# Performance work log

Hardware: AMD Instinct MI355X
Metric: run time of the kernel (lower is better)

Reference implementation:

```python
import jax, jax.numpy as jnp
import numpy as np

USER_NUM, ITEM_NUM, D, E, B = 50000, 20000, 64, 2_000_000, 16384
N = USER_NUM + ITEM_NUM


def setup_inputs() -> dict:
    key = jax.random.key(0)
    ks = jax.random.split(key, 20)
    return {
        "user_emb": jax.random.normal(ks[0], (USER_NUM, D), jnp.float32),
        "item_emb": jax.random.normal(ks[1], (ITEM_NUM, D), jnp.float32),
        "edge_row": jax.random.randint(ks[2], (E,), 0, N, jnp.int32),
        "edge_col": jax.random.randint(ks[3], (E,), 0, N, jnp.int32),
        "edge_val": jax.random.uniform(ks[4], (E,), jnp.float32),
        "Wg1": jax.random.normal(ks[5], (D, D), jnp.float32) * 0.05,
        "bg1": jax.random.normal(ks[6], (D,), jnp.float32) * 0.05,
        "Wg2": jax.random.normal(ks[7], (D, D), jnp.float32) * 0.05,
        "bg2": jax.random.normal(ks[8], (D,), jnp.float32) * 0.05,
        "W1": jax.random.normal(ks[9], (4 * D, D), jnp.float32) * 0.05,
        "b1": jax.random.normal(ks[10], (D,), jnp.float32) * 0.05,
        "W2": jax.random.normal(ks[11], (D, 32), jnp.float32) * 0.05,
        "b2": jax.random.normal(ks[12], (32,), jnp.float32) * 0.05,
        "W3": jax.random.normal(ks[13], (32, 1), jnp.float32) * 0.05,
        "b3": jax.random.normal(ks[14], (1,), jnp.float32) * 0.05,
        "userID": jax.random.randint(ks[15], (B,), 0, USER_NUM, jnp.int32),
        "itemID": jax.random.randint(ks[16], (B,), 0, ITEM_NUM, jnp.int32),
    }


def _spmm(row, col, val, x):
    # sparse [N,N] @ dense [N,D] via gather + segment_sum
    msgs = val[:, None] * x[col]  # [E, D]
    return jax.ops.segment_sum(msgs, row, num_segments=N)


def reference(user_emb, item_emb, edge_row, edge_col, edge_val,
              Wg1, bg1, Wg2, bg2, W1, b1, W2, b2, W3, b3, userID, itemID):
    features = jnp.concatenate([user_emb, item_emb], axis=0)  # [N, D]
    final = features
    # single GCN layer (layers=[64,64]); L1 = L + I so SpMM(L1,x) = SpMM(L,x) + x
    lx = _spmm(edge_row, edge_col, edge_val, features)
    lx2 = _spmm(edge_row, edge_col, edge_val, features * features)
    inter1 = (lx + features) @ Wg1 + bg1
    inter2 = lx2 @ Wg2 + bg2
    h = jax.nn.leaky_relu(inter1 + inter2, negative_slope=0.01)
    final = jnp.concatenate([final, h], axis=1)  # [N, 2D]

    u = final[userID]                     # [B, 2D]
    i = final[itemID + USER_NUM]          # [B, 2D]
    embed = jnp.concatenate([u, i], axis=1)  # [B, 4D]
    embed = jax.nn.relu(embed @ W1 + b1)
    embed = jax.nn.relu(embed @ W2 + b2)
    embed = embed @ W3 + b3
    return embed.reshape(-1)
```

## Files before the change

kernel.cpp:

```cpp
#include <hip/hip_runtime.h>
#include <hip/hip_bf16.h>

#define USER_NUM 50000
#define ITEM_NUM 20000
#define NNODE    70000
#define DD       64
#define CHUNK    1024
#define NCHUNK   ((NNODE + CHUNK - 1) / CHUNK)
#define GROWS    (NNODE / 8)
#define APB      2048
#define EPT      8
#define NS2      128
#define NB3      16
#define T_CAP    32768
#define NCHUNK2  (T_CAP / CHUNK)
#define GCAP     327680
#define RT       16

__device__ __forceinline__ const float* feat_row(const float* __restrict__ ue,
                                                 const float* __restrict__ ie, int n) {
    return (n < USER_NUM) ? (ue + (size_t)n * DD)
                          : (ie + (size_t)(n - USER_NUM) * DD);
}


__global__ __launch_bounds__(256) void zero_kernel(int* __restrict__ cnt2,
                                                   int* __restrict__ tmask,
                                                   int* __restrict__ gcur) {
    const int tid    = blockIdx.x * 256 + (int)threadIdx.x;
    const int stride = gridDim.x * 256;
    for (int i = tid; i < T_CAP; i += stride) cnt2[i] = 0;
    for (int i = tid; i < NNODE; i += stride) tmask[i] = 0;
    if (tid < 8) gcur[tid] = tid * GCAP;
}


__global__ __launch_bounds__(256) void mark_kernel(const int* __restrict__ uid,
                                                   const int* __restrict__ iid,
                                                   int* __restrict__ tmask, int B) {
    const int stride = gridDim.x * blockDim.x;
    for (int s = blockIdx.x * blockDim.x + threadIdx.x; s < B; s += stride) {
        tmask[uid[s]] = 1;
        tmask[USER_NUM + iid[s]] = 1;
    }
}


__global__ __launch_bounds__(256) void chunksum_kernel(const int* __restrict__ arr,
                                                       int* __restrict__ csum, int N) {
    __shared__ int red[4];
    const int c = blockIdx.x;
    const int t = threadIdx.x;
    int s = 0;
#pragma unroll
    for (int i = 0; i < 4; ++i) {
        const int idx = c * CHUNK + t + 256 * i;
        s += (idx < N) ? arr[idx] : 0;
    }
#pragma unroll
    for (int off = 32; off; off >>= 1) s += __shfl_down(s, off);
    if ((t & 63) == 0) red[t >> 6] = s;
    __syncthreads();
    if (t == 0) csum[c] = red[0] + red[1] + red[2] + red[3];
}

__global__ __launch_bounds__(128) void scan_small_kernel(const int* __restrict__ csum,
                                                         int* __restrict__ coff,
                                                         int NC) {
    __shared__ int s[128];
    const int t = threadIdx.x;
    const int v = (t < NC) ? csum[t] : 0;
    s[t] = v;
    __syncthreads();
    for (int off = 1; off < 128; off <<= 1) {
        const int val = s[t];
        const int add = (t >= off) ? s[t - off] : 0;
        __syncthreads();
        s[t] = val + add;
        __syncthreads();
    }
    if (t < NC) coff[t] = s[t] - v;
}

__global__ __launch_bounds__(256) void fill_flags_kernel(
    const int* __restrict__ tmask, const int* __restrict__ coff,
    int* __restrict__ cmapx, int* __restrict__ nodes, int* __restrict__ meta,
    int* __restrict__ gslot) {
    __shared__ int sp[256];
    const int c  = blockIdx.x;
    const int t  = threadIdx.x;
    const int g0 = c * CHUNK + t * 4;
    int v[4];
#pragma unroll
    for (int i = 0; i < 4; ++i) v[i] = (g0 + i < NNODE) ? tmask[g0 + i] : 0;
    const int s = ((v[0] + v[1]) + (v[2] + v[3]));
    sp[t] = s;
    __syncthreads();
    for (int off = 1; off < 256; off <<= 1) {
        const int val = sp[t];
        const int add = (t >= off) ? sp[t - off] : 0;
        __syncthreads();
        sp[t] = val + add;
        __syncthreads();
    }
    int run = coff[c] + sp[t] - s;
#pragma unroll
    for (int i = 0; i < 4; ++i) {
        const int g = g0 + i;
        if (g < NNODE) {
            cmapx[g] = v[i] ? run : -1;
            if (v[i]) nodes[run] = g;
            if (g == USER_NUM) meta[1] = run;
            if (g % GROWS == 0) gslot[g / GROWS] = run;
            run += v[i];
        } else if (g == NNODE) {
            meta[0] = run;
            gslot[8] = run;
        }
    }
    if (g0 + 4 == NNODE) { meta[0] = run; gslot[8] = run; }
}

__global__ __launch_bounds__(256) void fill_kernel(const int* __restrict__ cnt,
                                                   const int* __restrict__ coff,
                                                   int* __restrict__ base,
                                                   int* __restrict__ cursor, int N) {
    __shared__ int sp[256];
    const int c  = blockIdx.x;
    const int t  = threadIdx.x;
    const int g0 = c * CHUNK + t * 4;
    int v[4];
#pragma unroll
    for (int i = 0; i < 4; ++i) v[i] = (g0 + i < N) ? cnt[g0 + i] : 0;
    const int s = ((v[0] + v[1]) + (v[2] + v[3]));
    sp[t] = s;
    __syncthreads();
    for (int off = 1; off < 256; off <<= 1) {
        const int val = sp[t];
        const int add = (t >= off) ? sp[t - off] : 0;
        __syncthreads();
        sp[t] = val + add;
        __syncthreads();
    }
    int run = coff[c] + sp[t] - s;
#pragma unroll
    for (int i = 0; i < 4; ++i) {
        const int g = g0 + i;
        if (g < N) {
            base[g]   = run;
            cursor[g] = run;
            run += v[i];
        }
    }
    if (g0 + 4 == N) base[N] = run;
}


__global__ __launch_bounds__(256) void append_kernel(
    const int* __restrict__ erow, const int* __restrict__ ecol,
    const float* __restrict__ eval, const int* __restrict__ cmapx,
    int* __restrict__ gcur, int* __restrict__ grow, int2* __restrict__ gpair,
    int E) {
    __shared__ int lcnt[8];
    __shared__ int lbase[8];
    const int t = threadIdx.x;
    if (t < 8) lcnt[t] = 0;
    __syncthreads();
    const int e0 = blockIdx.x * APB + t;
    int sl[EPT], c[EPT], gr[EPT], rk[EPT];
    float v[EPT];
#pragma unroll
    for (int i = 0; i < EPT; ++i) {
        const int e = e0 + 256 * i;
        gr[i] = -1;
        if (e < E) {
            const int r = erow[e];
            const int slot = cmapx[r];
            if (slot >= 0) {
                sl[i] = slot;
                c[i]  = ecol[e];
                v[i]  = eval[e];
                gr[i] = (r * 8) / NNODE;
                rk[i] = atomicAdd(&lcnt[gr[i]], 1);
            }
        }
    }
    __syncthreads();
    if (t < 8 && lcnt[t] > 0) lbase[t] = atomicAdd(&gcur[t], lcnt[t]);
    __syncthreads();
#pragma unroll
    for (int i = 0; i < EPT; ++i) {
        if (gr[i] >= 0) {
            const int pos = lbase[gr[i]] + rk[i];
            grow[pos]  = sl[i];
            gpair[pos] = make_int2(c[i], __float_as_int(v[i]));
        }
    }
}


__global__ __launch_bounds__(256) void hist3_kernel(const int* __restrict__ grow,
                                                    const int* __restrict__ gcur,
                                                    const int* __restrict__ gslot,
                                                    int* __restrict__ cnt2) {
    __shared__ int hloc[GROWS];
    const int g    = blockIdx.x & 7;
    const int rank = blockIdx.x >> 3;
    const int slo  = gslot[g];
    const int span = gslot[g + 1] - slo;
    for (int i = threadIdx.x; i < span; i += 256) hloc[i] = 0;
    __syncthreads();
    const int hi = gcur[g];
    for (int i = g * GCAP + rank * 256 + (int)threadIdx.x; i < hi; i += NB3 * 256)
        atomicAdd(&hloc[grow[i] - slo], 1);
    __syncthreads();
    for (int i = threadIdx.x; i < span; i += 256) {
        const int v = hloc[i];
        if (v) atomicAdd(&cnt2[slo + i], v);
    }
}


__global__ __launch_bounds__(256) void scatter2_kernel(
    const int* __restrict__ grow, const int2* __restrict__ gpair,
    const int* __restrict__ gcur, int* __restrict__ cursor2,
    int2* __restrict__ epair) {
    const int g    = blockIdx.x & 7;
    const int rank = blockIdx.x >> 3;
    const int hi = gcur[g];
    for (int i = g * GCAP + rank * 256 + (int)threadIdx.x; i < hi; i += NS2 * 256) {
        const int slot = grow[i];
        const int pos = atomicAdd(&cursor2[slot], 1);
        epair[pos] = gpair[i];
    }
}


__global__ __launch_bounds__(256) void spmm_kernel(
    const float* __restrict__ ue, const float* __restrict__ ie,
    const int2* __restrict__ epair, const int* __restrict__ base2,
    const int* __restrict__ nodes, const int* __restrict__ meta,
    float* __restrict__ lx, float* __restrict__ lx2) {
    const int T = meta[0];
    const int lane = threadIdx.x & 63;
    int wv = (int)((blockIdx.x * blockDim.x + threadIdx.x) >> 6);
    wv = __builtin_amdgcn_readfirstlane(wv);
    const int nw = (int)((gridDim.x * blockDim.x) >> 6);
    for (int r = wv; r < T; r += nw) {
        const int jb = base2[r];
        const int je = base2[r + 1];
        float acc1 = 0.f, acc2 = 0.f;
        int j = jb;
        for (; j + 8 <= je; j += 8) {
            int2 p[8];
#pragma unroll
            for (int t = 0; t < 8; ++t) p[t] = epair[j + t];
            float f[8];
#pragma unroll
            for (int t = 0; t < 8; ++t) f[t] = feat_row(ue, ie, p[t].x)[lane];
#pragma unroll
            for (int t = 0; t < 8; ++t) {
                const float v = __int_as_float(p[t].y);
                acc1 = fmaf(v, f[t], acc1);
                acc2 = fmaf(v * f[t], f[t], acc2);
            }
        }
        for (; j + 4 <= je; j += 4) {
            int2 p[4];
#pragma unroll
            for (int t = 0; t < 4; ++t) p[t] = epair[j + t];
            float f[4];
#pragma unroll
            for (int t = 0; t < 4; ++t) f[t] = feat_row(ue, ie, p[t].x)[lane];
#pragma unroll
            for (int t = 0; t < 4; ++t) {
                const float v = __int_as_float(p[t].y);
                acc1 = fmaf(v, f[t], acc1);
                acc2 = fmaf(v * f[t], f[t], acc2);
            }
        }
        for (; j < je; ++j) {
            const int2 p = epair[j];
            const float f = feat_row(ue, ie, p.x)[lane];
            const float v = __int_as_float(p.y);
            acc1 = fmaf(v, f, acc1);
            acc2 = fmaf(v * f, f, acc2);
        }
        const int n = nodes[r];
        lx [(size_t)r * DD + lane] = acc1 + feat_row(ue, ie, n)[lane];
        lx2[(size_t)r * DD + lane] = acc2;
    }
}


__global__ __launch_bounds__(256) void xform_fused_kernel(
    const float* __restrict__ lx, const float* __restrict__ lx2,
    const float* __restrict__ ue, const float* __restrict__ ie,
    const float* __restrict__ Wg1, const float* __restrict__ Wg2,
    const float* __restrict__ bg1, const float* __restrict__ bg2,
    const float* __restrict__ W1, const float* __restrict__ b1,
    float* __restrict__ part,
    const int* __restrict__ nodes, const int* __restrict__ meta, int nTilesU) {
    const int Tu = meta[1];
    const int T  = meta[0];
    const bool isU   = (int)blockIdx.x < nTilesU;
    const int tileIx = isU ? blockIdx.x : (blockIdx.x - nTilesU);
    const int start  = isU ? 0  : Tu;
    const int lim    = isU ? Tu : T;
    const int tb     = start + tileIx * RT;
    if (tb >= lim) return;
    const float* fb = isU ? ue : ie;

    __shared__ float sXa[RT * DD];
    __shared__ float sXb[RT * DD];
    __shared__ float sP [RT * DD];
    const int t     = threadIdx.x;
    const int lane  = t & 63;
    const int w     = t >> 6;
    const int khalf = (w & 1) * 32;
    const int rhalf = (w >> 1) * (RT / 2);

    float wva[32], wvb[32];
#pragma unroll
    for (int k = 0; k < 32; ++k) {
        wva[k] = Wg1[(khalf + k) * DD + lane];
        wvb[k] = Wg2[(khalf + k) * DD + lane];
    }

    float4* sXav = (float4*)sXa;
    float4* sXbv = (float4*)sXb;
    float4* sPv  = (float4*)sP;
#pragma unroll
    for (int i = 0; i < RT / 16; ++i) {
        const int f4  = t + 256 * i;
        const int row = f4 >> 4;
        const int c   = f4 & 15;
        const int g   = min(tb + row, lim - 1);
        sXav[f4] = ((const float4*)(lx  + (size_t)g * DD))[c];
        sXbv[f4] = ((const float4*)(lx2 + (size_t)g * DD))[c];
        sPv[f4]  = make_float4(0.f, 0.f, 0.f, 0.f);
    }
    __syncthreads();

#pragma unroll 2
    for (int r = 0; r < RT / 2; ++r) {
        const int row = rhalf + r;
        const float* ra = &sXa[row * DD + khalf];
        const float* rb = &sXb[row * DD + khalf];
        float o0 = 0.f, o1 = 0.f, o2 = 0.f, o3 = 0.f;
#pragma unroll
        for (int q = 0; q < 8; ++q) {
            const float4 qa = *(const float4*)(ra + 4 * q);
            const float4 qb = *(const float4*)(rb + 4 * q);
            o0 = fmaf(qa.x, wva[4 * q + 0], o0);
            o1 = fmaf(qa.y, wva[4 * q + 1], o1);
            o0 = fmaf(qa.z, wva[4 * q + 2], o0);
            o1 = fmaf(qa.w, wva[4 * q + 3], o1);
            o2 = fmaf(qb.x, wvb[4 * q + 0], o2);
            o3 = fmaf(qb.y, wvb[4 * q + 1], o3);
            o2 = fmaf(qb.z, wvb[4 * q + 2], o2);
            o3 = fmaf(qb.w, wvb[4 * q + 3], o3);
        }
        atomicAdd(&sP[row * DD + lane], (o0 + o1) + (o2 + o3));
    }
    __syncthreads();

#pragma unroll
    for (int i = 0; i < RT / 16; ++i) {
        const int f4  = t + 256 * i;
        const int row = f4 >> 4;
        const int c   = f4 & 15;
        float4 v = sPv[f4];
        const float4 ba = ((const float4*)bg1)[c];
        const float4 bb = ((const float4*)bg2)[c];
        v.x += ba.x + bb.x; v.y += ba.y + bb.y;
        v.z += ba.z + bb.z; v.w += ba.w + bb.w;
        v.x = (v.x > 0.f) ? v.x : 0.01f * v.x;
        v.y = (v.y > 0.f) ? v.y : 0.01f * v.y;
        v.z = (v.z > 0.f) ? v.z : 0.01f * v.z;
        v.w = (v.w > 0.f) ? v.w : 0.01f * v.w;
        sXav[f4] = v;
        sPv[f4]  = make_float4(0.f, 0.f, 0.f, 0.f);
        const int g = min(tb + row, lim - 1);
        int n = nodes[g];
        if (!isU) n -= USER_NUM;
        sXbv[f4] = ((const float4*)(fb + (size_t)n * DD))[c];
    }

    const float* W1a = W1 + (isU ? 0 : 2 * DD * DD);
    const float* W1b = W1a + DD * DD;
#pragma unroll
    for (int k = 0; k < 32; ++k) {
        wva[k] = W1b[(khalf + k) * DD + lane];
        wvb[k] = W1a[(khalf + k) * DD + lane];
    }
    __syncthreads();

#pragma unroll 2
    for (int r = 0; r < RT / 2; ++r) {
        const int row = rhalf + r;
        const float* ra = &sXa[row * DD + khalf];
        const float* rb = &sXb[row * DD + khalf];
        float o0 = 0.f, o1 = 0.f, o2 = 0.f, o3 = 0.f;
#pragma unroll
        for (int q = 0; q < 8; ++q) {
            const float4 qa = *(const float4*)(ra + 4 * q);
            const float4 qb = *(const float4*)(rb + 4 * q);
            o0 = fmaf(qa.x, wva[4 * q + 0], o0);
            o1 = fmaf(qa.y, wva[4 * q + 1], o1);
            o0 = fmaf(qa.z, wva[4 * q + 2], o0);
            o1 = fmaf(qa.w, wva[4 * q + 3], o1);
            o2 = fmaf(qb.x, wvb[4 * q + 0], o2);
            o3 = fmaf(qb.y, wvb[4 * q + 1], o3);
            o2 = fmaf(qb.z, wvb[4 * q + 2], o2);
            o3 = fmaf(qb.w, wvb[4 * q + 3], o3);
        }
        atomicAdd(&sP[row * DD + lane], (o0 + o1) + (o2 + o3));
    }
    __syncthreads();

    float4* outv = (float4*)part;
#pragma unroll
    for (int i = 0; i < RT / 16; ++i) {
        const int f4  = t + 256 * i;
        const int row = f4 >> 4;
        const int c   = f4 & 15;
        const int g   = tb + row;
        float4 v = sPv[f4];
        if (isU) {
            const float4 b = ((const float4*)b1)[c];
            v.x += b.x; v.y += b.y; v.z += b.z; v.w += b.w;
        }
        if (g < lim) outv[(size_t)g * 16 + c] = v;
    }
}


__global__ __launch_bounds__(256) void mlp_kernel(
    const float* __restrict__ part, const int* __restrict__ cmapx,
    const float* __restrict__ W2, const float* __restrict__ b2,
    const float* __restrict__ W3, const float* __restrict__ b3,
    const int* __restrict__ uid, const int* __restrict__ iid,
    float* __restrict__ out, int B) {
    __shared__ float sW2[DD * 32];
    __shared__ float sW3[32];
    for (int i = threadIdx.x; i < DD * 32; i += 256) sW2[i] = W2[i];
    if (threadIdx.x < 32) sW3[threadIdx.x] = W3[threadIdx.x];
    __syncthreads();
    const int lane = threadIdx.x & 63;
    const int wave = (int)((blockIdx.x * blockDim.x + threadIdx.x) >> 6);
    const int nw   = (int)((gridDim.x * blockDim.x) >> 6);
    const float bias2 = b2[lane & 31];
    const float w3v   = sW3[lane & 31];
    const float bias3 = b3[0];
    for (int s = wave; s < B; s += nw) {
        const int su = cmapx[uid[s]];
        const int si = cmapx[USER_NUM + iid[s]];
        const float pu = part[(size_t)su * DD + lane];
        const float pi = part[(size_t)si * DD + lane];
        const float x  = pu + pi;
        const float o1 = (x > 0.f) ? x : 0.f;
        float acc_a = bias2, acc_b = 0.f;
#pragma unroll
        for (int k = 0; k < DD; k += 2) {
            acc_a = fmaf(__shfl(o1, k),     sW2[k * 32 + (lane & 31)],       acc_a);
            acc_b = fmaf(__shfl(o1, k + 1), sW2[(k + 1) * 32 + (lane & 31)], acc_b);
        }
        const float a2 = acc_a + acc_b;
        const float o2 = (a2 > 0.f) ? a2 : 0.f;
        float p = o2 * w3v;
        p += __shfl_xor(p, 1);
        p += __shfl_xor(p, 2);
        p += __shfl_xor(p, 4);
        p += __shfl_xor(p, 8);
        p += __shfl_xor(p, 16);
        if (lane == 0) out[s] = p + bias3;
    }
}

extern "C" void kernel_launch(void* const* d_in, const int* in_sizes, int n_in,
                              void* d_out, int out_size, void* d_ws, size_t ws_size,
                              hipStream_t stream) {
    const float* ue   = (const float*)d_in[0];
    const float* ie   = (const float*)d_in[1];
    const int*   erow = (const int*)d_in[2];
    const int*   ecol = (const int*)d_in[3];
    const float* evalp= (const float*)d_in[4];
    const float* Wg1  = (const float*)d_in[5];
    const float* bg1  = (const float*)d_in[6];
    const float* Wg2  = (const float*)d_in[7];
    const float* bg2  = (const float*)d_in[8];
    const float* W1   = (const float*)d_in[9];
    const float* b1   = (const float*)d_in[10];
    const float* W2   = (const float*)d_in[11];
    const float* b2   = (const float*)d_in[12];
    const float* W3   = (const float*)d_in[13];
    const float* b3   = (const float*)d_in[14];
    const int*   uid  = (const int*)d_in[15];
    const int*   iid  = (const int*)d_in[16];
    float* out = (float*)d_out;

    const int E = in_sizes[2];
    const int B = in_sizes[15];

    const int TU_MAX = (B < USER_NUM) ? B : USER_NUM;
    const int TI_MAX = (B < ITEM_NUM) ? B : ITEM_NUM;
    const int nTilesU = (TU_MAX + RT - 1) / RT;
    const int nTilesI = (TI_MAX + RT - 1) / RT;

    char* ws = (char*)d_ws;
    const size_t ndc = (size_t)T_CAP * DD;
    float* lx    = (float*)ws;
    float* lx2   = lx + ndc;
    float* part  = lx2 + ndc;
    int*   grow  = (int*)ws;
    int2*  gpair = (int2*)(ws + 11u * 1024 * 1024);
    char*  tail  = ws + 32u * 1024 * 1024;
    int2*  epair = (int2*)tail;
    int*   mi    = (int*)(tail + (size_t)E * sizeof(int2));
    int*   cnt2    = mi;
    int*   cursor2 = cnt2 + T_CAP;
    int*   base2   = cursor2 + T_CAP;
    int*   tmask   = base2 + T_CAP + 1;
    int*   cmapx   = tmask + NNODE;
    int*   nodes   = cmapx + NNODE;
    int*   csum    = nodes + T_CAP;
    int*   coff    = csum + 128;
    int*   gcur    = coff + 128;
    int*   meta    = gcur + 8;
    int*   gslot   = meta + 8;

    zero_kernel<<<512, 256, 0, stream>>>(cnt2, tmask, gcur);
    mark_kernel<<<(B + 255) / 256, 256, 0, stream>>>(uid, iid, tmask, B);
    chunksum_kernel<<<NCHUNK, 256, 0, stream>>>(tmask, csum, NNODE);
    scan_small_kernel<<<1, 128, 0, stream>>>(csum, coff, NCHUNK);
    fill_flags_kernel<<<NCHUNK, 256, 0, stream>>>(tmask, coff, cmapx, nodes,
                                                  meta, gslot);
    append_kernel<<<(E + APB - 1) / APB, 256, 0, stream>>>(
        erow, ecol, evalp, cmapx, gcur, grow, gpair, E);
    hist3_kernel<<<8 * NB3, 256, 0, stream>>>(grow, gcur, gslot, cnt2);
    chunksum_kernel<<<NCHUNK2, 256, 0, stream>>>(cnt2, csum, T_CAP);
    scan_small_kernel<<<1, 128, 0, stream>>>(csum, coff, NCHUNK2);
    fill_kernel<<<NCHUNK2, 256, 0, stream>>>(cnt2, coff, base2, cursor2, T_CAP);
    scatter2_kernel<<<8 * NS2, 256, 0, stream>>>(grow, gpair, gcur, cursor2, epair);
    spmm_kernel<<<4096, 256, 0, stream>>>(ue, ie, epair, base2, nodes, meta,
                                          lx, lx2);

    xform_fused_kernel<<<nTilesU + nTilesI, 256, 0, stream>>>(
        lx, lx2, ue, ie, Wg1, Wg2, bg1, bg2, W1, b1, part, nodes, meta, nTilesU);

    mlp_kernel<<<1024, 256, 0, stream>>>(part, cmapx, W2, b2, W3, b3,
                                         uid, iid, out, B);
}
```

Measured before the change: 200.9 us.

## Rewrite transform kernel as one-row-per-thread register GEMM with uniform weight loads

Replaces the 16-row tile transform kernel, which used shared-memory atomics for split-K reduction, with a 64-thread block in which each thread owns one node row and keeps a 64-float accumulator in registers. Weight reads are wave-uniform, so they can be served as scalar or broadcast loads, and the LDS atomics and most barriers go away. The cost is very high register pressure from the 64 accumulators plus 16 float4 feature values. Each thread also reads its lx/lx2 row with strided scalar loads, which are uncoalesced across lanes, and the smaller grid of 64-thread blocks lowers occupancy.

```diff
diff --git a/kernel.cpp b/kernel.cpp
--- a/kernel.cpp
+++ b/kernel.cpp
@@ -15,7 +15,6 @@
 #define T_CAP    32768
 #define NCHUNK2  (T_CAP / CHUNK)
 #define GCAP     327680
-#define RT       16
 
 __device__ __forceinline__ const float* feat_row(const float* __restrict__ ue,
                                                  const float* __restrict__ ie, int n) {
@@ -293,145 +292,97 @@
 }
 
 
-__global__ __launch_bounds__(256) void xform_fused_kernel(
+__global__ __launch_bounds__(64) void xform_reg_kernel(
     const float* __restrict__ lx, const float* __restrict__ lx2,
     const float* __restrict__ ue, const float* __restrict__ ie,
     const float* __restrict__ Wg1, const float* __restrict__ Wg2,
     const float* __restrict__ bg1, const float* __restrict__ bg2,
     const float* __restrict__ W1, const float* __restrict__ b1,
     float* __restrict__ part,
-    const int* __restrict__ nodes, const int* __restrict__ meta, int nTilesU) {
-    const int Tu = meta[1];
-    const int T  = meta[0];
-    const bool isU   = (int)blockIdx.x < nTilesU;
-    const int tileIx = isU ? blockIdx.x : (blockIdx.x - nTilesU);
-    const int start  = isU ? 0  : Tu;
-    const int lim    = isU ? Tu : T;
-    const int tb     = start + tileIx * RT;
-    if (tb >= lim) return;
+    const int* __restrict__ nodes, const int* __restrict__ meta) {
+    __shared__ float f_s[64 * 65];
+    __shared__ float h_s[64 * 65];
+    const int Tu  = meta[1];
+    const int T   = meta[0];
+    const int nTu = (Tu + 63) >> 6;
+    const int tile = blockIdx.x;
+    bool isU;
+    int rowBase, lim;
+    if (tile < nTu) {
+        isU = true;  rowBase = tile * 64;              lim = Tu;
+    } else {
+        isU = false; rowBase = Tu + (tile - nTu) * 64; lim = T;
+        if (rowBase >= T) return;
+    }
+    const int lane = threadIdx.x;
+    const int g    = rowBase + lane;
+    const int gc   = min(g, lim - 1);
+
+    int n = nodes[gc];
+    if (!isU) n -= USER_NUM;
     const float* fb = isU ? ue : ie;
-
-    __shared__ float sXa[RT * DD];
-    __shared__ float sXb[RT * DD];
-    __shared__ float sP [RT * DD];
-    const int t     = threadIdx.x;
-    const int lane  = t & 63;
-    const int w     = t >> 6;
-    const int khalf = (w & 1) * 32;
-    const int rhalf = (w >> 1) * (RT / 2);
-
-    float wva[32], wvb[32];
-#pragma unroll
-    for (int k = 0; k < 32; ++k) {
-        wva[k] = Wg1[(khalf + k) * DD + lane];
-        wvb[k] = Wg2[(khalf + k) * DD + lane];
-    }
-
-    float4* sXav = (float4*)sXa;
-    float4* sXbv = (float4*)sXb;
-    float4* sPv  = (float4*)sP;
-#pragma unroll
-    for (int i = 0; i < RT / 16; ++i) {
-        const int f4  = t + 256 * i;
-        const int row = f4 >> 4;
-        const int c   = f4 & 15;
-        const int g   = min(tb + row, lim - 1);
-        sXav[f4] = ((const float4*)(lx  + (size_t)g * DD))[c];
-        sXbv[f4] = ((const float4*)(lx2 + (size_t)g * DD))[c];
-        sPv[f4]  = make_float4(0.f, 0.f, 0.f, 0.f);
-    }
-    __syncthreads();
-
+    const float4* frow = (const float4*)(fb + (size_t)n * DD);
+    float4 fr[16];
+#pragma unroll
+    for (int q = 0; q < 16; ++q) fr[q] = frow[q];
+
+    float acc[64];
+#pragma unroll
+    for (int j = 0; j < 64; ++j) acc[j] = 0.f;
+    const float* xrow = lx  + (size_t)gc * DD;
+    const float* yrow = lx2 + (size_t)gc * DD;
 #pragma unroll 2
-    for (int r = 0; r < RT / 2; ++r) {
-        const int row = rhalf + r;
-        const float* ra = &sXa[row * DD + khalf];
-        const float* rb = &sXb[row * DD + khalf];
-        float o0 = 0.f, o1 = 0.f, o2 = 0.f, o3 = 0.f;
-#pragma unroll
-        for (int q = 0; q < 8; ++q) {
-            const float4 qa = *(const float4*)(ra + 4 * q);
-            const float4 qb = *(const float4*)(rb + 4 * q);
-            o0 = fmaf(qa.x, wva[4 * q + 0], o0);
-            o1 = fmaf(qa.y, wva[4 * q + 1], o1);
-            o0 = fmaf(qa.z, wva[4 * q + 2], o0);
-            o1 = fmaf(qa.w, wva[4 * q + 3], o1);
-            o2 = fmaf(qb.x, wvb[4 * q + 0], o2);
-            o3 = fmaf(qb.y, wvb[4 * q + 1], o3);
-            o2 = fmaf(qb.z, wvb[4 * q + 2], o2);
-            o3 = fmaf(qb.w, wvb[4 * q + 3], o3);
-        }
-        atomicAdd(&sP[row * DD + lane], (o0 + o1) + (o2 + o3));
-    }
-    __syncthreads();
-
-#pragma unroll
-    for (int i = 0; i < RT / 16; ++i) {
-        const int f4  = t + 256 * i;
-        const int row = f4 >> 4;
-        const int c   = f4 & 15;
-        float4 v = sPv[f4];
-        const float4 ba = ((const float4*)bg1)[c];
-        const float4 bb = ((const float4*)bg2)[c];
-        v.x += ba.x + bb.x; v.y += ba.y + bb.y;
-        v.z += ba.z + bb.z; v.w += ba.w + bb.w;
-        v.x = (v.x > 0.f) ? v.x : 0.01f * v.x;
-        v.y = (v.y > 0.f) ? v.y : 0.01f * v.y;
-        v.z = (v.z > 0.f) ? v.z : 0.01f * v.z;
-        v.w = (v.w > 0.f) ? v.w : 0.01f * v.w;
-        sXav[f4] = v;
-        sPv[f4]  = make_float4(0.f, 0.f, 0.f, 0.f);
-        const int g = min(tb + row, lim - 1);
-        int n = nodes[g];
-        if (!isU) n -= USER_NUM;
-        sXbv[f4] = ((const float4*)(fb + (size_t)n * DD))[c];
+    for (int k = 0; k < 64; ++k) {
+        const float xk = xrow[k];
+        const float yk = yrow[k];
+        const float* w1k = Wg1 + k * DD;
+        const float* w2k = Wg2 + k * DD;
+#pragma unroll
+        for (int j = 0; j < 64; ++j)
+            acc[j] = fmaf(xk, w1k[j], fmaf(yk, w2k[j], acc[j]));
+    }
+
+#pragma unroll
+    for (int j = 0; j < 64; ++j) {
+        const float x = acc[j] + bg1[j] + bg2[j];
+        h_s[lane * 65 + j] = (x > 0.f) ? x : 0.01f * x;
+        acc[j] = 0.f;
+    }
+#pragma unroll
+    for (int q = 0; q < 16; ++q) {
+        const int b = lane * 65 + 4 * q;
+        f_s[b]     = fr[q].x;
+        f_s[b + 1] = fr[q].y;
+        f_s[b + 2] = fr[q].z;
+        f_s[b + 3] = fr[q].w;
     }
 
     const float* W1a = W1 + (isU ? 0 : 2 * DD * DD);
     const float* W1b = W1a + DD * DD;
-#pragma unroll
-    for (int k = 0; k < 32; ++k) {
-        wva[k] = W1b[(khalf + k) * DD + lane];
-        wvb[k] = W1a[(khalf + k) * DD + lane];
-    }
-    __syncthreads();
-
 #pragma unroll 2
-    for (int r = 0; r < RT / 2; ++r) {
-        const int row = rhalf + r;
-        const float* ra = &sXa[row * DD + khalf];
-        const float* rb = &sXb[row * DD + khalf];
-        float o0 = 0.f, o1 = 0.f, o2 = 0.f, o3 = 0.f;
-#pragma unroll
-        for (int q = 0; q < 8; ++q) {
-            const float4 qa = *(const float4*)(ra + 4 * q);
-            const float4 qb = *(const float4*)(rb + 4 * q);
-            o0 = fmaf(qa.x, wva[4 * q + 0], o0);
-            o1 = fmaf(qa.y, wva[4 * q + 1], o1);
-            o0 = fmaf(qa.z, wva[4 * q + 2], o0);
-            o1 = fmaf(qa.w, wva[4 * q + 3], o1);
-            o2 = fmaf(qb.x, wvb[4 * q + 0], o2);
-            o3 = fmaf(qb.y, wvb[4 * q + 1], o3);
-            o2 = fmaf(qb.z, wvb[4 * q + 2], o2);
-            o3 = fmaf(qb.w, wvb[4 * q + 3], o3);
-        }
-        atomicAdd(&sP[row * DD + lane], (o0 + o1) + (o2 + o3));
-    }
-    __syncthreads();
-
-    float4* outv = (float4*)part;
-#pragma unroll
-    for (int i = 0; i < RT / 16; ++i) {
-        const int f4  = t + 256 * i;
-        const int row = f4 >> 4;
-        const int c   = f4 & 15;
-        const int g   = tb + row;
-        float4 v = sPv[f4];
-        if (isU) {
-            const float4 b = ((const float4*)b1)[c];
-            v.x += b.x; v.y += b.y; v.z += b.z; v.w += b.w;
-        }
-        if (g < lim) outv[(size_t)g * 16 + c] = v;
+    for (int k = 0; k < 64; ++k) {
+        const float fk = f_s[lane * 65 + k];
+        const float hk = h_s[lane * 65 + k];
+        const float* wak = W1a + k * DD;
+        const float* wbk = W1b + k * DD;
+#pragma unroll
+        for (int j = 0; j < 64; ++j)
+            acc[j] = fmaf(fk, wak[j], fmaf(hk, wbk[j], acc[j]));
+    }
+
+    if (g < lim) {
+        float4* orow = (float4*)(part + (size_t)g * DD);
+#pragma unroll
+        for (int q = 0; q < 16; ++q) {
+            float4 v;
+            v.x = acc[4 * q];     v.y = acc[4 * q + 1];
+            v.z = acc[4 * q + 2]; v.w = acc[4 * q + 3];
+            if (isU) {
+                v.x += b1[4 * q];     v.y += b1[4 * q + 1];
+                v.z += b1[4 * q + 2]; v.w += b1[4 * q + 3];
+            }
+            orow[q] = v;
+        }
     }
 }
 
@@ -505,8 +456,7 @@
 
     const int TU_MAX = (B < USER_NUM) ? B : USER_NUM;
     const int TI_MAX = (B < ITEM_NUM) ? B : ITEM_NUM;
-    const int nTilesU = (TU_MAX + RT - 1) / RT;
-    const int nTilesI = (TI_MAX + RT - 1) / RT;
+    const int nTiles = (TU_MAX + 63) / 64 + (TI_MAX + 63) / 64;
 
     char* ws = (char*)d_ws;
     const size_t ndc = (size_t)T_CAP * DD;
@@ -546,8 +496,8 @@
     spmm_kernel<<<4096, 256, 0, stream>>>(ue, ie, epair, base2, nodes, meta,
                                           lx, lx2);
 
-    xform_fused_kernel<<<nTilesU + nTilesI, 256, 0, stream>>>(
-        lx, lx2, ue, ie, Wg1, Wg2, bg1, bg2, W1, b1, part, nodes, meta, nTilesU);
+    xform_reg_kernel<<<nTiles, 64, 0, stream>>>(
+        lx, lx2, ue, ie, Wg1, Wg2, bg1, bg2, W1, b1, part, nodes, meta);
 
     mlp_kernel<<<1024, 256, 0, stream>>>(part, cmapx, W2, b2, W3, b3,
                                          uid, iid, out, B);
```

Measured after the change: 260.5 us. 1.3x slower.
